# Kernel tuning notes

Measured on AMD Instinct MI355X. Metric: run time of the kernel, lower is better.

## Reference

```python
import jax, jax.numpy as jnp
import numpy as np

B, N, D = 8, 4096, 256
H = 8
DH = D // H          # 32 per-head dim
M = 256              # number of random features
DEPTH = 4
HID = 4 * D          # mlp hidden
EPS = 1e-6


def layernorm(x, g, b):
    mu = jnp.mean(x, axis=-1, keepdims=True)
    var = jnp.mean(jnp.square(x - mu), axis=-1, keepdims=True)
    return (x - mu) * jax.lax.rsqrt(var + EPS) * g + b


def _phi(t, proj, is_query):
    # t: (B,H,N,DH), proj: (M,DH) -> (B,H,N,M) nonnegative softmax-kernel features
    nrm = DH ** -0.25
    td = t * nrm
    u = jnp.einsum('bhnd,md->bhnm', td, proj)
    diag = 0.5 * jnp.sum(td * td, axis=-1, keepdims=True)
    if is_query:
        mx = jnp.max(u, axis=-1, keepdims=True)
    else:
        mx = jnp.max(u, axis=(-2, -1), keepdims=True)
    return (jnp.exp(u - diag - mx) + 1e-4) / jnp.sqrt(jnp.asarray(M, t.dtype))


def performer_attn(h, Wqkv, Wproj, bproj, proj):
    # h: (B,N,D)
    qkv = h @ Wqkv                                   # (B,N,3D)
    q, k, v = jnp.split(qkv, 3, axis=-1)
    to_heads = lambda t: t.reshape(B, N, H, DH).transpose(0, 2, 1, 3)
    q, k, v = to_heads(q), to_heads(k), to_heads(v)  # (B,H,N,DH)
    qp = _phi(q, proj, True)                         # (B,H,N,M)
    kp = _phi(k, proj, False)                        # (B,H,N,M)
    kv = jnp.einsum('bhnm,bhnd->bhmd', kp, v)        # (B,H,M,DH) linear-time context
    z = 1.0 / (jnp.einsum('bhnm,bhm->bhn', qp, kp.sum(axis=2)) + 1e-6)
    out = jnp.einsum('bhnm,bhmd->bhnd', qp, kv) * z[..., None]
    out = out.transpose(0, 2, 1, 3).reshape(B, N, D)
    return out @ Wproj + bproj


def mlp(h, W1, b1, W2, b2):
    return jax.nn.gelu(h @ W1 + b1, approximate=False) @ W2 + b2


def setup_inputs() -> dict:
    key = jax.random.key(0)
    ks = jax.random.split(key, 10)
    inp = {
        'x': jax.random.normal(ks[0], (B, N, D), jnp.float32),
        'pos_emb': 0.02 * jax.random.normal(ks[1], (N, D), jnp.float32),
        'g1n': jnp.ones((D,), jnp.float32),
        'b1n': jnp.zeros((D,), jnp.float32),
        'g2n': jnp.ones((D,), jnp.float32),
        'b2n': jnp.zeros((D,), jnp.float32),
        'Wqkv': 0.02 * jax.random.normal(ks[2], (DEPTH, D, 3 * D), jnp.float32),
        'Wproj': 0.02 * jax.random.normal(ks[3], (DEPTH, D, D), jnp.float32),
        'bproj': jnp.zeros((DEPTH, D), jnp.float32),
        'W1': 0.02 * jax.random.normal(ks[4], (DEPTH, D, HID), jnp.float32),
        'b1m': jnp.zeros((DEPTH, HID), jnp.float32),
        'W2': 0.02 * jax.random.normal(ks[5], (DEPTH, HID, D), jnp.float32),
        'b2m': jnp.zeros((DEPTH, D), jnp.float32),
        'proj_mat': jax.random.normal(ks[6], (DEPTH, M, DH), jnp.float32),
    }
    return inp


def reference(x, pos_emb, g1n, b1n, g2n, b2n, Wqkv, Wproj, bproj, W1, b1m, W2, b2m, proj_mat):
    h = x + pos_emb[None]
    for l in range(DEPTH):  # small fixed depth
        h = h + performer_attn(layernorm(h, g1n, b1n), Wqkv[l], Wproj[l], bproj[l], proj_mat[l])
        h = h + mlp(layernorm(h, g2n, b2n), W1[l], b1m[l], W2[l], b2m[l])
    return h
```

## Files before the change

### kernel.cpp

```cpp
#include <hip/hip_runtime.h>
#include <hip/hip_bf16.h>
#include <math.h>

#define B 8
#define N 4096
#define D 256
#define H 8
#define DH 32
#define M 256
#define DEPTH 4
#define HID 1024
#define NRM 0.4204482076268573f

typedef __attribute__((ext_vector_type(8))) short short8;
typedef __attribute__((ext_vector_type(4))) float f32x4;

static __device__ __forceinline__ unsigned short f2bf(float f) {
    __hip_bfloat16 h = __float2bfloat16(f);
    return __builtin_bit_cast(unsigned short, h);
}
static __device__ __forceinline__ float bfu2f(unsigned short u) {
    unsigned int x = ((unsigned int)u) << 16;
    return __builtin_bit_cast(float, x);
}

__global__ void add_pos_kernel(const float* __restrict__ x, const float* __restrict__ pos,
                               float* __restrict__ h) {
    int i = blockIdx.x * 256 + threadIdx.x;
    int nd = i % (N * D);
    h[i] = x[i] + pos[nd];
}

__global__ void projbf_kernel(const float* __restrict__ in, unsigned short* __restrict__ out) {
    int i = blockIdx.x * 256 + threadIdx.x;
    out[i] = f2bf(in[i]);
}

__global__ __launch_bounds__(256) void wtrans_kernel(const float* __restrict__ in,
                                                     unsigned short* __restrict__ out,
                                                     int Kd, int Nd, int slim) {
    __shared__ float tl[32][33];
    int n0 = blockIdx.x * 32, k0 = blockIdx.y * 32;
    int t = threadIdx.x;
    int kk = t >> 3, c4 = (t & 7) * 4;
    float4 v = *reinterpret_cast<const float4*>(&in[(size_t)(k0 + kk) * Nd + n0 + c4]);
    tl[kk][c4 + 0] = v.x; tl[kk][c4 + 1] = v.y; tl[kk][c4 + 2] = v.z; tl[kk][c4 + 3] = v.w;
    __syncthreads();
    int nn = t >> 3, k4 = (t & 7) * 4;
    float sc = (n0 + nn < slim) ? NRM : 1.0f;
    ushort4 o;
    o.x = f2bf(tl[k4 + 0][nn] * sc); o.y = f2bf(tl[k4 + 1][nn] * sc);
    o.z = f2bf(tl[k4 + 2][nn] * sc); o.w = f2bf(tl[k4 + 3][nn] * sc);
    *reinterpret_cast<ushort4*>(&out[(size_t)(n0 + nn) * Kd + k0 + k4]) = o;
}

__global__ __launch_bounds__(256) void ln_kernel(const float* __restrict__ in,
                                                 const float* __restrict__ g,
                                                 const float* __restrict__ bb,
                                                 unsigned short* __restrict__ out) {
    int wave = threadIdx.x >> 6, lane = threadIdx.x & 63;
    long row = (long)blockIdx.x * 4 + wave;
    float4 v = reinterpret_cast<const float4*>(in + row * D)[lane];
    float s = v.x + v.y + v.z + v.w;
#pragma unroll
    for (int o = 32; o >= 1; o >>= 1) s += __shfl_xor(s, o);
    float mu = s * (1.0f / D);
    float d0 = v.x - mu, d1 = v.y - mu, d2 = v.z - mu, d3 = v.w - mu;
    float ss = d0 * d0 + d1 * d1 + d2 * d2 + d3 * d3;
#pragma unroll
    for (int o = 32; o >= 1; o >>= 1) ss += __shfl_xor(ss, o);
    float inv = rsqrtf(ss * (1.0f / D) + 1e-6f);
    float4 gv = reinterpret_cast<const float4*>(g)[lane];
    float4 bv = reinterpret_cast<const float4*>(bb)[lane];
    ushort4 o4;
    o4.x = f2bf(d0 * inv * gv.x + bv.x);
    o4.y = f2bf(d1 * inv * gv.y + bv.y);
    o4.z = f2bf(d2 * inv * gv.z + bv.z);
    o4.w = f2bf(d3 * inv * gv.w + bv.w);
    *reinterpret_cast<ushort4*>(&out[row * D + lane * 4]) = o4;
}

template <bool BIAS, bool GELU_ACT, bool RESID, bool OUT16>
__global__ __launch_bounds__(256) void mgemm_kernel(const unsigned short* __restrict__ A,
                                                    const unsigned short* __restrict__ Bt,
                                                    const float* __restrict__ bias,
                                                    float* __restrict__ C,
                                                    unsigned short* __restrict__ O16,
                                                    int K, int Nc) {
    __shared__ short Als[128][40];
    __shared__ short Bls[128][40];
    int t = threadIdx.x;
    int l = t & 63, w = t >> 6;
    int wr = w >> 1, wc = w & 1;
    int nwg = gridDim.x * gridDim.y;
    int bid = blockIdx.y * gridDim.x + blockIdx.x;
    int lgid = (bid & 7) * (nwg >> 3) + (bid >> 3);
    int bx = lgid % gridDim.x;
    int by = lgid / gridDim.x;
    long m0 = (long)by * 128;
    int n0 = bx * 128;
    int lr = l & 15;
    int lg = l >> 4;
    int kp8 = lg * 8;
    int srow = t >> 2, skoff = (t & 3) * 8;

    const unsigned short* Ap0 = &A[(size_t)(m0 + srow) * K + skoff];
    const unsigned short* Ap1 = Ap0 + (size_t)64 * K;
    const unsigned short* Bp0 = &Bt[(size_t)(n0 + srow) * K + skoff];
    const unsigned short* Bp1 = Bp0 + (size_t)64 * K;

    short8 ra0 = *reinterpret_cast<const short8*>(Ap0);
    short8 ra1 = *reinterpret_cast<const short8*>(Ap1);
    short8 rb0 = *reinterpret_cast<const short8*>(Bp0);
    short8 rb1 = *reinterpret_cast<const short8*>(Bp1);

    f32x4 acc[4][4];
#pragma unroll
    for (int i = 0; i < 4; i++)
#pragma unroll
        for (int j = 0; j < 4; j++) acc[i][j] = (f32x4){0.f, 0.f, 0.f, 0.f};

    for (int k0 = 0; k0 < K; k0 += 32) {
        *reinterpret_cast<short8*>(&Als[srow][skoff]) = ra0;
        *reinterpret_cast<short8*>(&Als[srow + 64][skoff]) = ra1;
        *reinterpret_cast<short8*>(&Bls[srow][skoff]) = rb0;
        *reinterpret_cast<short8*>(&Bls[srow + 64][skoff]) = rb1;
        __syncthreads();
        if (k0 + 32 < K) {
            ra0 = *reinterpret_cast<const short8*>(Ap0 + k0 + 32);
            ra1 = *reinterpret_cast<const short8*>(Ap1 + k0 + 32);
            rb0 = *reinterpret_cast<const short8*>(Bp0 + k0 + 32);
            rb1 = *reinterpret_cast<const short8*>(Bp1 + k0 + 32);
        }
        short8 a[4], b[4];
#pragma unroll
        for (int i = 0; i < 4; i++)
            a[i] = *reinterpret_cast<const short8*>(&Als[wr * 64 + i * 16 + lr][kp8]);
#pragma unroll
        for (int j = 0; j < 4; j++)
            b[j] = *reinterpret_cast<const short8*>(&Bls[wc * 64 + j * 16 + lr][kp8]);
#pragma unroll
        for (int i = 0; i < 4; i++)
#pragma unroll
            for (int j = 0; j < 4; j++)
                acc[i][j] = __builtin_amdgcn_mfma_f32_16x16x32_bf16(b[j], a[i], acc[i][j], 0, 0, 0);
        __syncthreads();
    }

    float4 bias4[4];
    if (BIAS) {
#pragma unroll
        for (int j = 0; j < 4; j++)
            bias4[j] = *reinterpret_cast<const float4*>(&bias[n0 + wc * 64 + j * 16 + lg * 4]);
    }
#pragma unroll
    for (int i = 0; i < 4; i++) {
        long grow = m0 + wr * 64 + i * 16 + lr;
#pragma unroll
        for (int j = 0; j < 4; j++) {
            int gcol = n0 + wc * 64 + j * 16 + lg * 4;
            f32x4 v = acc[i][j];
            if (BIAS) {
                v[0] += bias4[j].x; v[1] += bias4[j].y; v[2] += bias4[j].z; v[3] += bias4[j].w;
            }
            if (GELU_ACT) {
#pragma unroll
                for (int r = 0; r < 4; r++)
                    v[r] = 0.5f * v[r] * (1.0f + erff(v[r] * 0.70710678118654752f));
            }
            if (OUT16) {
                short4 o;
                o.x = (short)f2bf(v[0]); o.y = (short)f2bf(v[1]);
                o.z = (short)f2bf(v[2]); o.w = (short)f2bf(v[3]);
                *reinterpret_cast<short4*>(&O16[grow * Nc + gcol]) = o;
            } else if (RESID) {
                float4 c0 = *reinterpret_cast<const float4*>(&C[grow * Nc + gcol]);
                c0.x += v[0]; c0.y += v[1]; c0.z += v[2]; c0.w += v[3];
                *reinterpret_cast<float4*>(&C[grow * Nc + gcol]) = c0;
            } else {
                float4 c0 = {v[0], v[1], v[2], v[3]};
                *reinterpret_cast<float4*>(&C[grow * Nc + gcol]) = c0;
            }
        }
    }
}

#define KV_P 16
#define KV_ROWS (N / KV_P)
#define PSZ 8484
__global__ __launch_bounds__(256) void kv_kernel(const unsigned short* __restrict__ qkv16,
                                                 const unsigned short* __restrict__ projbf,
                                                 float* __restrict__ kvp) {
    __shared__ __align__(16) unsigned short kp_sT[256][72];
    __shared__ __align__(16) unsigned short vT_s[32][72];
    __shared__ float red[4];
    __shared__ float asumred[4][256];
    __shared__ float vred[256][4];
    int t = threadIdx.x;
    int l = t & 63, w = t >> 6;
    int lr = l & 15, lg = l >> 4;
    int bh = blockIdx.x, b = bh >> 3, h = bh & 7;
    int n0 = blockIdx.y * KV_ROWS;

    f32x4 kvacc[4][2];
#pragma unroll
    for (int mf = 0; mf < 4; mf++)
#pragma unroll
        for (int dd = 0; dd < 2; dd++) kvacc[mf][dd] = (f32x4){0.f, 0.f, 0.f, 0.f};
    float asum_p[16];
#pragma unroll
    for (int f = 0; f < 16; f++) asum_p[f] = 0.f;
    float4 vs4 = {0.f, 0.f, 0.f, 0.f};
    float Lm = -1e30f;

    for (int c = 0; c < KV_ROWS / 64; c++) {
        size_t kbase = ((size_t)(b * N) + n0 + c * 64 + w * 16 + lr) * 768 + 256 + h * 32 + lg * 8;
        short8 aq = *reinterpret_cast<const short8*>(qkv16 + kbase);
        float sq = 0.f;
#pragma unroll
        for (int e = 0; e < 8; e++) {
            float xx = bfu2f((unsigned short)aq[e]);
            sq += xx * xx;
        }
        sq += __shfl_xor(sq, 16);
        sq += __shfl_xor(sq, 32);
        f32x4 ua[16];
#pragma unroll
        for (int f = 0; f < 16; f++) {
            short8 bq = *reinterpret_cast<const short8*>(projbf + (f * 16 + lr) * 32 + lg * 8);
            ua[f] = __builtin_amdgcn_mfma_f32_16x16x32_bf16(aq, bq, (f32x4){0.f, 0.f, 0.f, 0.f}, 0, 0, 0);
        }
        float cm = -1e30f;
#pragma unroll
        for (int f = 0; f < 16; f++)
#pragma unroll
            for (int r = 0; r < 4; r++) cm = fmaxf(cm, ua[f][r]);
#pragma unroll
        for (int o = 1; o < 64; o <<= 1) cm = fmaxf(cm, __shfl_xor(cm, o));
        if (l == 0) red[w] = cm;
        __syncthreads();
        float bm = fmaxf(fmaxf(red[0], red[1]), fmaxf(red[2], red[3]));
        if (bm > Lm) {
            float sc = __expf(Lm - bm);
#pragma unroll
            for (int mf = 0; mf < 4; mf++)
#pragma unroll
                for (int dd = 0; dd < 2; dd++) {
                    kvacc[mf][dd][0] *= sc; kvacc[mf][dd][1] *= sc;
                    kvacc[mf][dd][2] *= sc; kvacc[mf][dd][3] *= sc;
                }
#pragma unroll
            for (int f = 0; f < 16; f++) asum_p[f] *= sc;
            Lm = bm;
        }
        float dgr[4];
#pragma unroll
        for (int r = 0; r < 4; r++) dgr[r] = 0.5f * __shfl(sq, lg * 4 + r);
#pragma unroll
        for (int f = 0; f < 16; f++) {
#pragma unroll
            for (int r = 0; r < 4; r++) {
                float p = __expf(ua[f][r] - dgr[r] - Lm);
                asum_p[f] += p;
                kp_sT[f * 16 + lr][w * 16 + lg * 4 + r] = f2bf(p);
            }
        }
#pragma unroll
        for (int ii = 0; ii < 2; ii++) {
            int idx = t + ii * 256;
            int nn = idx >> 3, dz = (idx & 7) * 4;
            const unsigned short* vp =
                qkv16 + ((size_t)(b * N) + n0 + c * 64 + nn) * 768 + 512 + h * 32 + dz;
            short4 vv = *reinterpret_cast<const short4*>(vp);
            float v0 = bfu2f((unsigned short)vv.x), v1 = bfu2f((unsigned short)vv.y);
            float v2 = bfu2f((unsigned short)vv.z), v3 = bfu2f((unsigned short)vv.w);
            vs4.x += v0; vs4.y += v1; vs4.z += v2; vs4.w += v3;
            vT_s[dz + 0][nn] = (unsigned short)vv.x; vT_s[dz + 1][nn] = (unsigned short)vv.y;
            vT_s[dz + 2][nn] = (unsigned short)vv.z; vT_s[dz + 3][nn] = (unsigned short)vv.w;
        }
        __syncthreads();
#pragma unroll
        for (int ks = 0; ks < 2; ks++) {
            short8 bv0 = *reinterpret_cast<const short8*>(&vT_s[lr][ks * 32 + lg * 8]);
            short8 bv1 = *reinterpret_cast<const short8*>(&vT_s[16 + lr][ks * 32 + lg * 8]);
#pragma unroll
            for (int mf = 0; mf < 4; mf++) {
                short8 am = *reinterpret_cast<const short8*>(&kp_sT[w * 64 + mf * 16 + lr][ks * 32 + lg * 8]);
                kvacc[mf][0] = __builtin_amdgcn_mfma_f32_16x16x32_bf16(am, bv0, kvacc[mf][0], 0, 0, 0);
                kvacc[mf][1] = __builtin_amdgcn_mfma_f32_16x16x32_bf16(am, bv1, kvacc[mf][1], 0, 0, 0);
            }
        }
    }
#pragma unroll
    for (int f = 0; f < 16; f++) {
        asum_p[f] += __shfl_xor(asum_p[f], 16);
        asum_p[f] += __shfl_xor(asum_p[f], 32);
    }
    if (l < 16) {
#pragma unroll
        for (int f = 0; f < 16; f++) asumred[w][f * 16 + l] = asum_p[f];
    }
    vred[t][0] = vs4.x; vred[t][1] = vs4.y; vred[t][2] = vs4.z; vred[t][3] = vs4.w;
    __syncthreads();
    size_t base = ((size_t)bh * KV_P + blockIdx.y) * PSZ;
#pragma unroll
    for (int mf = 0; mf < 4; mf++)
#pragma unroll
        for (int dd = 0; dd < 2; dd++)
#pragma unroll
            for (int r = 0; r < 4; r++) {
                int m = w * 64 + mf * 16 + lg * 4 + r;
                int d = dd * 16 + lr;
                kvp[base + m * 32 + d] = kvacc[mf][dd][r];
            }
    {
        float s = asumred[0][t] + asumred[1][t] + asumred[2][t] + asumred[3][t];
        kvp[base + 8192 + t] = s;
    }
    if (t < 32) {
        int f4g = t >> 2, cc = t & 3;
        float s = 0.f;
#pragma unroll
        for (int g = 0; g < 32; g++) s += vred[g * 8 + f4g][cc];
        kvp[base + 8448 + t] = s;
    }
    if (t == 0) kvp[base + 8480] = Lm;
}

__global__ __launch_bounds__(256) void kv_combine_kernel(const float* __restrict__ kvp,
                                                         unsigned short* __restrict__ kvTb,
                                                         float* __restrict__ ksumf) {
    __shared__ float vst[32];
    int t = threadIdx.x;
    int bh = blockIdx.x;
    size_t base0 = (size_t)bh * KV_P * PSZ;
    float Lp[KV_P];
    float gm = -1e30f;
#pragma unroll
    for (int p = 0; p < KV_P; p++) {
        Lp[p] = kvp[base0 + p * PSZ + 8480];
        gm = fmaxf(gm, Lp[p]);
    }
    if (t < 32) {
        float s = 0.f;
#pragma unroll
        for (int p = 0; p < KV_P; p++) s += kvp[base0 + p * PSZ + 8448 + t];
        vst[t] = s;
    }
    __syncthreads();
    float4 av[8];
#pragma unroll
    for (int d4 = 0; d4 < 8; d4++) av[d4] = (float4){0.f, 0.f, 0.f, 0.f};
    float S = 0.f;
#pragma unroll
    for (int p = 0; p < KV_P; p++) {
        float e = __expf(Lp[p] - gm);
        size_t pb = base0 + p * PSZ;
#pragma unroll
        for (int d4 = 0; d4 < 8; d4++) {
            float4 a = *reinterpret_cast<const float4*>(&kvp[pb + t * 32 + d4 * 4]);
            av[d4].x += e * a.x; av[d4].y += e * a.y; av[d4].z += e * a.z; av[d4].w += e * a.w;
        }
        S += e * kvp[pb + 8192 + t];
    }
#pragma unroll
    for (int d4 = 0; d4 < 8; d4++) {
        float o0 = (av[d4].x + 1e-4f * vst[d4 * 4 + 0]) * 0.0625f;
        float o1 = (av[d4].y + 1e-4f * vst[d4 * 4 + 1]) * 0.0625f;
        float o2 = (av[d4].z + 1e-4f * vst[d4 * 4 + 2]) * 0.0625f;
        float o3 = (av[d4].w + 1e-4f * vst[d4 * 4 + 3]) * 0.0625f;
        kvTb[((size_t)bh * 32 + d4 * 4 + 0) * 256 + t] = f2bf(o0);
        kvTb[((size_t)bh * 32 + d4 * 4 + 1) * 256 + t] = f2bf(o1);
        kvTb[((size_t)bh * 32 + d4 * 4 + 2) * 256 + t] = f2bf(o2);
        kvTb[((size_t)bh * 32 + d4 * 4 + 3) * 256 + t] = f2bf(o3);
    }
    ksumf[bh * 256 + t] = (S + 1e-4f * (float)N) * 0.0625f;
}

#define ATT_TILES 8
__global__ __launch_bounds__(256) void attn_kernel(const unsigned short* __restrict__ qkv16,
                                                   const unsigned short* __restrict__ projbf,
                                                   const unsigned short* __restrict__ kvTb,
                                                   const float* __restrict__ ksumf,
                                                   unsigned short* __restrict__ attn16) {
    __shared__ __align__(16) unsigned short qp_s[64 * 256];
    int t = threadIdx.x;
    int l = t & 63, w = t >> 6;
    int lr = l & 15, lg = l >> 4;
    int bh = blockIdx.x, b = bh >> 3, h = bh & 7;
    int swz = (lr & 7) << 3;
    int row = w * 16 + lr;

    const unsigned short* kvb = kvTb + (size_t)bh * 32 * 256;
    short8 kva0[8], kva1[8];
#pragma unroll
    for (int k0 = 0; k0 < 8; k0++) {
        kva0[k0] = *reinterpret_cast<const short8*>(kvb + (size_t)lr * 256 + k0 * 32 + lg * 8);
        kva1[k0] = *reinterpret_cast<const short8*>(kvb + (size_t)(16 + lr) * 256 + k0 * 32 + lg * 8);
    }

    int tile0 = blockIdx.y * ATT_TILES;
    size_t qstep = (size_t)64 * 768;
    size_t qbase = ((size_t)(b * N) + tile0 * 64 + w * 16 + lr) * 768 + h * 32 + lg * 8;
    short8 qf = *reinterpret_cast<const short8*>(qkv16 + qbase);

    for (int tl = 0; tl < ATT_TILES; tl++) {
        short8 qfn = qf;
        if (tl < ATT_TILES - 1)
            qfn = *reinterpret_cast<const short8*>(qkv16 + qbase + (size_t)(tl + 1) * qstep);

        float sq = 0.f;
#pragma unroll
        for (int e = 0; e < 8; e++) {
            float xx = bfu2f((unsigned short)qf[e]);
            sq += xx * xx;
        }
        sq += __shfl_xor(sq, 16);
        sq += __shfl_xor(sq, 32);
        float dg = 0.5f * sq;

        f32x4 ua[16];
#pragma unroll
        for (int f = 0; f < 16; f++) {
            short8 bq = *reinterpret_cast<const short8*>(projbf + (f * 16 + lr) * 32 + lg * 8);
            ua[f] = __builtin_amdgcn_mfma_f32_16x16x32_bf16(bq, qf, (f32x4){0.f, 0.f, 0.f, 0.f}, 0, 0, 0);
        }

        float mx = -1e30f;
#pragma unroll
        for (int f = 0; f < 16; f++)
#pragma unroll
            for (int r = 0; r < 4; r++) mx = fmaxf(mx, ua[f][r]);
        mx = fmaxf(mx, __shfl_xor(mx, 16));
        mx = fmaxf(mx, __shfl_xor(mx, 32));

        float zs = 0.f;
#pragma unroll
        for (int f = 0; f < 16; f++) {
            float4 ks4 = *reinterpret_cast<const float4*>(&ksumf[bh * 256 + f * 16 + lg * 4]);
            float p0 = (__expf(ua[f][0] - dg - mx) + 1e-4f) * 0.0625f;
            float p1 = (__expf(ua[f][1] - dg - mx) + 1e-4f) * 0.0625f;
            float p2 = (__expf(ua[f][2] - dg - mx) + 1e-4f) * 0.0625f;
            float p3 = (__expf(ua[f][3] - dg - mx) + 1e-4f) * 0.0625f;
            zs += p0 * ks4.x + p1 * ks4.y + p2 * ks4.z + p3 * ks4.w;
            short4 o;
            o.x = (short)f2bf(p0); o.y = (short)f2bf(p1);
            o.z = (short)f2bf(p2); o.w = (short)f2bf(p3);
            *reinterpret_cast<short4*>(&qp_s[row * 256 + ((f * 16 + lg * 4) ^ swz)]) = o;
        }
        zs += __shfl_xor(zs, 16);
        zs += __shfl_xor(zs, 32);
        float zf = 1.0f / (zs + 1e-6f);

        f32x4 oacc[2];
        oacc[0] = (f32x4){0.f, 0.f, 0.f, 0.f};
        oacc[1] = (f32x4){0.f, 0.f, 0.f, 0.f};
#pragma unroll
        for (int k0 = 0; k0 < 8; k0++) {
            short8 qpf = *reinterpret_cast<const short8*>(
                &qp_s[row * 256 + ((k0 * 32 + lg * 8) ^ swz)]);
            oacc[0] = __builtin_amdgcn_mfma_f32_16x16x32_bf16(kva0[k0], qpf, oacc[0], 0, 0, 0);
            oacc[1] = __builtin_amdgcn_mfma_f32_16x16x32_bf16(kva1[k0], qpf, oacc[1], 0, 0, 0);
        }
        size_t orow = ((size_t)(b * N) + (tile0 + tl) * 64 + w * 16 + lr) * 256 + h * 32;
#pragma unroll
        for (int dd = 0; dd < 2; dd++) {
            short4 o;
            o.x = (short)f2bf(oacc[dd][0] * zf);
            o.y = (short)f2bf(oacc[dd][1] * zf);
            o.z = (short)f2bf(oacc[dd][2] * zf);
            o.w = (short)f2bf(oacc[dd][3] * zf);
            *reinterpret_cast<short4*>(&attn16[orow + dd * 16 + lg * 4]) = o;
        }
        qf = qfn;
    }
}

extern "C" void kernel_launch(void* const* d_in, const int* in_sizes, int n_in,
                              void* d_out, int out_size, void* d_ws, size_t ws_size,
                              hipStream_t stream) {
    const float* x = (const float*)d_in[0];
    const float* pos = (const float*)d_in[1];
    const float* g1 = (const float*)d_in[2];
    const float* b1 = (const float*)d_in[3];
    const float* g2 = (const float*)d_in[4];
    const float* b2 = (const float*)d_in[5];
    const float* Wqkv = (const float*)d_in[6];
    const float* Wproj = (const float*)d_in[7];
    const float* bproj = (const float*)d_in[8];
    const float* W1 = (const float*)d_in[9];
    const float* b1m = (const float*)d_in[10];
    const float* W2 = (const float*)d_in[11];
    const float* b2m = (const float*)d_in[12];
    const float* projm = (const float*)d_in[13];

    float* h = (float*)d_out;
    char* p = (char*)d_ws;
    auto alloc = [&](size_t bytes) { char* r = p; p += (bytes + 255) & ~(size_t)255; return r; };
    unsigned short* wbf    = (unsigned short*)alloc((size_t)DEPTH * 786432 * 2);
    unsigned short* projb  = (unsigned short*)alloc((size_t)DEPTH * M * DH * 2);
    unsigned short* ln16   = (unsigned short*)alloc((size_t)B * N * D * 2);
    unsigned short* qkv16  = (unsigned short*)alloc((size_t)B * N * HID * 2);
    unsigned short* hid16  = qkv16;
    unsigned short* attn16 = (unsigned short*)alloc((size_t)B * N * D * 2);
    float* kvp             = (float*)alloc((size_t)64 * KV_P * PSZ * 4);
    unsigned short* kvTb   = (unsigned short*)alloc((size_t)64 * 32 * 256 * 2);
    float* ksumf           = (float*)alloc((size_t)64 * 256 * 4);

    for (int l = 0; l < DEPTH; l++) {
        size_t lb = (size_t)l * 786432;
        wtrans_kernel<<<dim3(768 / 32, 256 / 32), 256, 0, stream>>>(
            Wqkv + (size_t)l * D * 3 * D, wbf + lb + 0, 256, 768, 512);
        wtrans_kernel<<<dim3(256 / 32, 256 / 32), 256, 0, stream>>>(
            Wproj + (size_t)l * D * D, wbf + lb + 196608, 256, 256, 0);
        wtrans_kernel<<<dim3(1024 / 32, 256 / 32), 256, 0, stream>>>(
            W1 + (size_t)l * D * HID, wbf + lb + 262144, 256, 1024, 0);
        wtrans_kernel<<<dim3(256 / 32, 1024 / 32), 256, 0, stream>>>(
            W2 + (size_t)l * HID * D, wbf + lb + 524288, 1024, 256, 0);
    }
    projbf_kernel<<<DEPTH * M * DH / 256, 256, 0, stream>>>(projm, projb);

    add_pos_kernel<<<B * N * D / 256, 256, 0, stream>>>(x, pos, h);

    for (int l = 0; l < DEPTH; l++) {
        size_t lb = (size_t)l * 786432;
        const unsigned short* wqT = wbf + lb + 0;
        const unsigned short* wpT = wbf + lb + 196608;
        const unsigned short* w1T = wbf + lb + 262144;
        const unsigned short* w2T = wbf + lb + 524288;
        const float* bp = bproj + (size_t)l * D;
        const float* b1l = b1m + (size_t)l * HID;
        const float* b2l = b2m + (size_t)l * D;
        const unsigned short* prb = projb + (size_t)l * M * DH;

        ln_kernel<<<B * N / 4, 256, 0, stream>>>(h, g1, b1, ln16);
        mgemm_kernel<false, false, false, true><<<dim3(768 / 128, B * N / 128), 256, 0, stream>>>(
            ln16, wqT, nullptr, nullptr, qkv16, 256, 768);
        kv_kernel<<<dim3(B * H, KV_P), 256, 0, stream>>>(qkv16, prb, kvp);
        kv_combine_kernel<<<B * H, 256, 0, stream>>>(kvp, kvTb, ksumf);
        attn_kernel<<<dim3(B * H, (N / 64) / ATT_TILES), 256, 0, stream>>>(
            qkv16, prb, kvTb, ksumf, attn16);
        mgemm_kernel<true, false, true, false><<<dim3(256 / 128, B * N / 128), 256, 0, stream>>>(
            attn16, wpT, bp, h, nullptr, 256, 256);
        ln_kernel<<<B * N / 4, 256, 0, stream>>>(h, g2, b2, ln16);
        mgemm_kernel<true, true, false, true><<<dim3(1024 / 128, B * N / 128), 256, 0, stream>>>(
            ln16, w1T, b1l, nullptr, hid16, 256, 1024);
        mgemm_kernel<true, false, true, false><<<dim3(256 / 128, B * N / 128), 256, 0, stream>>>(
            hid16, w2T, b2l, h, nullptr, 1024, 256);
    }
}
```

Baseline: 1.031 ms.

## Fuse MLP GEMMs into one kernel, swizzle kv LDS, split kv combine

Adds a fused MLP kernel that keeps a 64-row LayerNorm tile in LDS, computes 128-wide hidden chunks with GELU into LDS, and accumulates the second GEMM plus residual directly. This removes the bf16 hidden activation round-trip through global memory and one launch per layer. It also replaces the padded transposed kp buffer in kv_kernel with an XOR-swizzled layout written as vector stores, and splits kv_combine across four times as many blocks for more parallelism. The fused MLP reads weights straight from global memory without LDS staging and runs only 512 blocks, so weight-reuse and occupancy may be worse than in the tiled GEMMs.

New measurement: 1.076 ms. 4.4% more time.

```diff
diff --git a/kernel.cpp b/kernel.cpp
--- a/kernel.cpp
+++ b/kernel.cpp
@@ -185,14 +185,116 @@
     }
 }
 
+__global__ __launch_bounds__(256) void mlp_fused_kernel(const unsigned short* __restrict__ ln16,
+                                                        const unsigned short* __restrict__ w1T,
+                                                        const unsigned short* __restrict__ w2T,
+                                                        const float* __restrict__ b1,
+                                                        const float* __restrict__ b2,
+                                                        float* __restrict__ hres) {
+    __shared__ __align__(16) unsigned short A_s[64][256];
+    __shared__ __align__(16) unsigned short t1_s[64][128];
+    int t = threadIdx.x;
+    int l = t & 63, w = t >> 6;
+    int lr = l & 15, lg = l >> 4;
+    long m0 = (long)blockIdx.x * 64;
+    int rsw = (lr & 7) << 3;
+
+    {
+        int r = t >> 2, c0 = (t & 3) * 64;
+        const unsigned short* src = ln16 + (size_t)(m0 + r) * 256 + c0;
+        int sw = (r & 7) << 3;
+#pragma unroll
+        for (int i = 0; i < 8; i++) {
+            short8 v = *reinterpret_cast<const short8*>(src + i * 8);
+            *reinterpret_cast<short8*>(&A_s[r][(c0 + i * 8) ^ sw]) = v;
+        }
+    }
+    __syncthreads();
+
+    f32x4 oacc[4][4];
+#pragma unroll
+    for (int i = 0; i < 4; i++)
+#pragma unroll
+        for (int j = 0; j < 4; j++) oacc[i][j] = (f32x4){0.f, 0.f, 0.f, 0.f};
+
+    for (int ch = 0; ch < HID / 128; ch++) {
+        f32x4 acc1[4][2];
+#pragma unroll
+        for (int mf = 0; mf < 4; mf++)
+#pragma unroll
+            for (int nh = 0; nh < 2; nh++) acc1[mf][nh] = (f32x4){0.f, 0.f, 0.f, 0.f};
+#pragma unroll
+        for (int ks = 0; ks < 8; ks++) {
+#pragma unroll
+            for (int nh = 0; nh < 2; nh++) {
+                short8 wf = *reinterpret_cast<const short8*>(
+                    &w1T[(size_t)(ch * 128 + w * 32 + nh * 16 + lr) * 256 + ks * 32 + lg * 8]);
+#pragma unroll
+                for (int mf = 0; mf < 4; mf++) {
+                    short8 af = *reinterpret_cast<const short8*>(
+                        &A_s[mf * 16 + lr][(ks * 32 + lg * 8) ^ rsw]);
+                    acc1[mf][nh] = __builtin_amdgcn_mfma_f32_16x16x32_bf16(wf, af, acc1[mf][nh], 0, 0, 0);
+                }
+            }
+        }
+        __syncthreads();
+#pragma unroll
+        for (int nh = 0; nh < 2; nh++) {
+            float4 b1v = *reinterpret_cast<const float4*>(&b1[ch * 128 + w * 32 + nh * 16 + lg * 4]);
+#pragma unroll
+            for (int mf = 0; mf < 4; mf++) {
+                f32x4 v = acc1[mf][nh];
+                v[0] += b1v.x; v[1] += b1v.y; v[2] += b1v.z; v[3] += b1v.w;
+#pragma unroll
+                for (int r = 0; r < 4; r++)
+                    v[r] = 0.5f * v[r] * (1.0f + erff(v[r] * 0.70710678118654752f));
+                short4 o;
+                o.x = (short)f2bf(v[0]); o.y = (short)f2bf(v[1]);
+                o.z = (short)f2bf(v[2]); o.w = (short)f2bf(v[3]);
+                *reinterpret_cast<short4*>(&t1_s[mf * 16 + lr][(w * 32 + nh * 16 + lg * 4) ^ rsw]) = o;
+            }
+        }
+        __syncthreads();
+#pragma unroll
+        for (int ks = 0; ks < 4; ks++) {
+#pragma unroll
+            for (int nf = 0; nf < 4; nf++) {
+                short8 wf = *reinterpret_cast<const short8*>(
+                    &w2T[(size_t)(w * 64 + nf * 16 + lr) * 1024 + ch * 128 + ks * 32 + lg * 8]);
+#pragma unroll
+                for (int mf = 0; mf < 4; mf++) {
+                    short8 tf = *reinterpret_cast<const short8*>(
+                        &t1_s[mf * 16 + lr][(ks * 32 + lg * 8) ^ rsw]);
+                    oacc[mf][nf] = __builtin_amdgcn_mfma_f32_16x16x32_bf16(wf, tf, oacc[mf][nf], 0, 0, 0);
+                }
+            }
+        }
+    }
+
+#pragma unroll
+    for (int nf = 0; nf < 4; nf++) {
+        float4 b2v = *reinterpret_cast<const float4*>(&b2[w * 64 + nf * 16 + lg * 4]);
+#pragma unroll
+        for (int mf = 0; mf < 4; mf++) {
+            long grow = m0 + mf * 16 + lr;
+            int gcol = w * 64 + nf * 16 + lg * 4;
+            f32x4 v = oacc[mf][nf];
+            float4 c0 = *reinterpret_cast<const float4*>(&hres[grow * 256 + gcol]);
+            c0.x += v[0] + b2v.x; c0.y += v[1] + b2v.y;
+            c0.z += v[2] + b2v.z; c0.w += v[3] + b2v.w;
+            *reinterpret_cast<float4*>(&hres[grow * 256 + gcol]) = c0;
+        }
+    }
+}
+
 #define KV_P 16
 #define KV_ROWS (N / KV_P)
 #define PSZ 8484
 __global__ __launch_bounds__(256) void kv_kernel(const unsigned short* __restrict__ qkv16,
                                                  const unsigned short* __restrict__ projbf,
                                                  float* __restrict__ kvp) {
-    __shared__ __align__(16) unsigned short kp_sT[256][72];
-    __shared__ __align__(16) unsigned short vT_s[32][72];
+    __shared__ __align__(16) unsigned short kp_s[256][64];
+    __shared__ __align__(16) unsigned short vT_s[32][66];
     __shared__ float red[4];
     __shared__ float asumred[4][256];
     __shared__ float vred[256][4];
@@ -201,6 +303,7 @@
     int lr = l & 15, lg = l >> 4;
     int bh = blockIdx.x, b = bh >> 3, h = bh & 7;
     int n0 = blockIdx.y * KV_ROWS;
+    int rsw = (lr & 7) << 3;
 
     f32x4 kvacc[4][2];
 #pragma unroll
@@ -256,14 +359,18 @@
         float dgr[4];
 #pragma unroll
         for (int r = 0; r < 4; r++) dgr[r] = 0.5f * __shfl(sq, lg * 4 + r);
+        int cbase = (w * 16 + lg * 4) ^ rsw;
 #pragma unroll
         for (int f = 0; f < 16; f++) {
-#pragma unroll
-            for (int r = 0; r < 4; r++) {
-                float p = __expf(ua[f][r] - dgr[r] - Lm);
-                asum_p[f] += p;
-                kp_sT[f * 16 + lr][w * 16 + lg * 4 + r] = f2bf(p);
-            }
+            float p0 = __expf(ua[f][0] - dgr[0] - Lm);
+            float p1 = __expf(ua[f][1] - dgr[1] - Lm);
+            float p2 = __expf(ua[f][2] - dgr[2] - Lm);
+            float p3 = __expf(ua[f][3] - dgr[3] - Lm);
+            asum_p[f] += p0 + p1 + p2 + p3;
+            short4 o;
+            o.x = (short)f2bf(p0); o.y = (short)f2bf(p1);
+            o.z = (short)f2bf(p2); o.w = (short)f2bf(p3);
+            *reinterpret_cast<short4*>(&kp_s[f * 16 + lr][cbase]) = o;
         }
 #pragma unroll
         for (int ii = 0; ii < 2; ii++) {
@@ -285,7 +392,8 @@
             short8 bv1 = *reinterpret_cast<const short8*>(&vT_s[16 + lr][ks * 32 + lg * 8]);
 #pragma unroll
             for (int mf = 0; mf < 4; mf++) {
-                short8 am = *reinterpret_cast<const short8*>(&kp_sT[w * 64 + mf * 16 + lr][ks * 32 + lg * 8]);
+                short8 am = *reinterpret_cast<const short8*>(
+                    &kp_s[w * 64 + mf * 16 + lr][(ks * 32 + lg * 8) ^ rsw]);
                 kvacc[mf][0] = __builtin_amdgcn_mfma_f32_16x16x32_bf16(am, bv0, kvacc[mf][0], 0, 0, 0);
                 kvacc[mf][1] = __builtin_amdgcn_mfma_f32_16x16x32_bf16(am, bv1, kvacc[mf][1], 0, 0, 0);
             }
@@ -332,7 +440,7 @@
                                                          float* __restrict__ ksumf) {
     __shared__ float vst[32];
     int t = threadIdx.x;
-    int bh = blockIdx.x;
+    int bh = blockIdx.x >> 2, mq = blockIdx.x & 3;
     size_t base0 = (size_t)bh * KV_P * PSZ;
     float Lp[KV_P];
     float gm = -1e30f;
@@ -348,33 +456,29 @@
         vst[t] = s;
     }
     __syncthreads();
-    float4 av[8];
-#pragma unroll
-    for (int d4 = 0; d4 < 8; d4++) av[d4] = (float4){0.f, 0.f, 0.f, 0.f};
+    int m = mq * 64 + (t >> 2);
+    int d0 = (t & 3) * 8;
+    float4 av0 = {0.f, 0.f, 0.f, 0.f}, av1 = {0.f, 0.f, 0.f, 0.f};
     float S = 0.f;
 #pragma unroll
     for (int p = 0; p < KV_P; p++) {
         float e = __expf(Lp[p] - gm);
         size_t pb = base0 + p * PSZ;
-#pragma unroll
-        for (int d4 = 0; d4 < 8; d4++) {
-            float4 a = *reinterpret_cast<const float4*>(&kvp[pb + t * 32 + d4 * 4]);
-            av[d4].x += e * a.x; av[d4].y += e * a.y; av[d4].z += e * a.z; av[d4].w += e * a.w;
-        }
-        S += e * kvp[pb + 8192 + t];
-    }
-#pragma unroll
-    for (int d4 = 0; d4 < 8; d4++) {
-        float o0 = (av[d4].x + 1e-4f * vst[d4 * 4 + 0]) * 0.0625f;
-        float o1 = (av[d4].y + 1e-4f * vst[d4 * 4 + 1]) * 0.0625f;
-        float o2 = (av[d4].z + 1e-4f * vst[d4 * 4 + 2]) * 0.0625f;
-        float o3 = (av[d4].w + 1e-4f * vst[d4 * 4 + 3]) * 0.0625f;
-        kvTb[((size_t)bh * 32 + d4 * 4 + 0) * 256 + t] = f2bf(o0);
-        kvTb[((size_t)bh * 32 + d4 * 4 + 1) * 256 + t] = f2bf(o1);
-        kvTb[((size_t)bh * 32 + d4 * 4 + 2) * 256 + t] = f2bf(o2);
-        kvTb[((size_t)bh * 32 + d4 * 4 + 3) * 256 + t] = f2bf(o3);
-    }
-    ksumf[bh * 256 + t] = (S + 1e-4f * (float)N) * 0.0625f;
+        float4 a = *reinterpret_cast<const float4*>(&kvp[pb + m * 32 + d0]);
+        float4 bq = *reinterpret_cast<const float4*>(&kvp[pb + m * 32 + d0 + 4]);
+        av0.x += e * a.x; av0.y += e * a.y; av0.z += e * a.z; av0.w += e * a.w;
+        av1.x += e * bq.x; av1.y += e * bq.y; av1.z += e * bq.z; av1.w += e * bq.w;
+        if ((t & 3) == 0) S += e * kvp[pb + 8192 + m];
+    }
+    float o[8];
+    o[0] = av0.x; o[1] = av0.y; o[2] = av0.z; o[3] = av0.w;
+    o[4] = av1.x; o[5] = av1.y; o[6] = av1.z; o[7] = av1.w;
+#pragma unroll
+    for (int j = 0; j < 8; j++) {
+        float v = (o[j] + 1e-4f * vst[d0 + j]) * 0.0625f;
+        kvTb[((size_t)bh * 32 + d0 + j) * 256 + m] = f2bf(v);
+    }
+    if ((t & 3) == 0) ksumf[bh * 256 + m] = (S + 1e-4f * (float)N) * 0.0625f;
 }
 
 #define ATT_TILES 8
@@ -500,8 +604,7 @@
     unsigned short* wbf    = (unsigned short*)alloc((size_t)DEPTH * 786432 * 2);
     unsigned short* projb  = (unsigned short*)alloc((size_t)DEPTH * M * DH * 2);
     unsigned short* ln16   = (unsigned short*)alloc((size_t)B * N * D * 2);
-    unsigned short* qkv16  = (unsigned short*)alloc((size_t)B * N * HID * 2);
-    unsigned short* hid16  = qkv16;
+    unsigned short* qkv16  = (unsigned short*)alloc((size_t)B * N * 3 * D * 2);
     unsigned short* attn16 = (unsigned short*)alloc((size_t)B * N * D * 2);
     float* kvp             = (float*)alloc((size_t)64 * KV_P * PSZ * 4);
     unsigned short* kvTb   = (unsigned short*)alloc((size_t)64 * 32 * 256 * 2);
@@ -537,15 +640,12 @@
         mgemm_kernel<false, false, false, true><<<dim3(768 / 128, B * N / 128), 256, 0, stream>>>(
             ln16, wqT, nullptr, nullptr, qkv16, 256, 768);
         kv_kernel<<<dim3(B * H, KV_P), 256, 0, stream>>>(qkv16, prb, kvp);
-        kv_combine_kernel<<<B * H, 256, 0, stream>>>(kvp, kvTb, ksumf);
+        kv_combine_kernel<<<B * H * 4, 256, 0, stream>>>(kvp, kvTb, ksumf);
         attn_kernel<<<dim3(B * H, (N / 64) / ATT_TILES), 256, 0, stream>>>(
             qkv16, prb, kvTb, ksumf, attn16);
         mgemm_kernel<true, false, true, false><<<dim3(256 / 128, B * N / 128), 256, 0, stream>>>(
             attn16, wpT, bp, h, nullptr, 256, 256);
         ln_kernel<<<B * N / 4, 256, 0, stream>>>(h, g2, b2, ln16);
-        mgemm_kernel<true, true, false, true><<<dim3(1024 / 128, B * N / 128), 256, 0, stream>>>(
-            ln16, w1T, b1l, nullptr, hid16, 256, 1024);
-        mgemm_kernel<true, false, true, false><<<dim3(256 / 128, B * N / 128), 256, 0, stream>>>(
-            hid16, w2T, b2l, h, nullptr, 1024, 256);
-    }
-}
+        mlp_fused_kernel<<<B * N / 64, 256, 0, stream>>>(ln16, w1T, w2T, b1l, b2l, h);
+    }
+}
```
